# Performance work log

Hardware: AMD Instinct MI355X
Metric: run time of the kernel (lower is better)

The kernel has to match this reference:

```python
import jax, jax.numpy as jnp
import numpy as np

N_NODES = 100000
N_EDGES = 1600000
NUM_GRAPHS = 128
IN_DIM, HID, NCLS = 128, 64, 10


def setup_inputs() -> dict:
    key = jax.random.key(0)
    ks = jax.random.split(key, 12)
    inp = {
        'x': jax.random.normal(ks[0], (N_NODES, IN_DIM), jnp.float32),
        'edge_index': jax.random.randint(ks[1], (2, N_EDGES), 0, N_NODES),
        'edge_weight': jax.random.uniform(ks[2], (N_EDGES,), jnp.float32),
        'batch': jnp.sort(jax.random.randint(ks[3], (N_NODES,), 0, NUM_GRAPHS)),
        'W1': jax.random.normal(ks[4], (IN_DIM, HID), jnp.float32) * 0.05,
        'b1': jnp.zeros((HID,), jnp.float32),
        'W2': jax.random.normal(ks[5], (HID, HID), jnp.float32) * 0.05,
        'b2': jnp.zeros((HID,), jnp.float32),
        'Wc1': jax.random.normal(ks[6], (HID, HID // 2), jnp.float32) * 0.05,
        'bc1': jnp.zeros((HID // 2,), jnp.float32),
        'Wc2': jax.random.normal(ks[7], (HID // 2, NCLS), jnp.float32) * 0.05,
        'bc2': jnp.zeros((NCLS,), jnp.float32),
    }
    return inp


def _gcn_conv(x, row, col, ew, W, b, n):
    # PyG GCNConv: add self-loops (weight 1), symmetric normalization,
    # transform then aggregate: out[col] += norm * (xW)[row]
    loop = jnp.arange(n)
    r = jnp.concatenate([row, loop])
    c = jnp.concatenate([col, loop])
    w = jnp.concatenate([ew, jnp.ones((n,), ew.dtype)])
    deg = jax.ops.segment_sum(w, c, num_segments=n)
    dinv = jnp.where(deg > 0, jax.lax.rsqrt(deg), 0.0)
    norm = dinv[r] * w * dinv[c]          # [E+N]
    h = x @ W                              # [N, out]
    msg = h[r] * norm[:, None]             # [E+N, out]
    out = jax.ops.segment_sum(msg, c, num_segments=n)
    return out + b


def reference(x, edge_index, edge_weight, batch, W1, b1, W2, b2, Wc1, bc1, Wc2, bc2):
    n = x.shape[0]
    row, col = edge_index[0], edge_index[1]
    h = jax.nn.relu(_gcn_conv(x, row, col, edge_weight, W1, b1, n))
    # dropout p=0.5 is identity in eval mode
    h = jax.nn.relu(_gcn_conv(h, row, col, edge_weight, W2, b2, n))
    # global mean pool over batch indices
    sums = jax.ops.segment_sum(h, batch, num_segments=NUM_GRAPHS)
    cnts = jax.ops.segment_sum(jnp.ones((n,), h.dtype), batch, num_segments=NUM_GRAPHS)
    pooled = sums / jnp.clip(cnts, 1.0)[:, None]   # [G, HID]
    z = jax.nn.relu(pooled @ Wc1 + bc1)
    return z @ Wc2 + bc2                            # [G, NCLS]
```

## Files before the change

### kernel.cpp

```cpp
#include <hip/hip_runtime.h>
#include <hip/hip_fp16.h>


#define TPB 256
#define FIX_SCALE 16777216.0f
#define BKT_BITS 8
#define PART_BLOCKS 256

typedef _Float16 f16x8 __attribute__((ext_vector_type(8)));
typedef float f32x4 __attribute__((ext_vector_type(4)));

__device__ __forceinline__ int lower_bound_i(const int* __restrict__ a, int n, int key) {
    int lo = 0, hi = n;
    while (lo < hi) {
        int mid = (lo + hi) >> 1;
        if (a[mid] < key) lo = mid + 1; else hi = mid;
    }
    return lo;
}

__global__ __launch_bounds__(256) void k_histA(const int* __restrict__ col, int E, int CH,
                                               int K, int* __restrict__ bh,
                                               const float* __restrict__ W1,
                                               const float* __restrict__ W2,
                                               __half* __restrict__ Wt1,
                                               __half* __restrict__ Wt2) {
    __shared__ int hist[512];
    int b = blockIdx.x, t = threadIdx.x;
    if (b == 0) {
        for (int i = t; i < 64 * 128; i += 256) {
            int c = i >> 7, k = i & 127;
            Wt1[i] = (__half)W1[k * 64 + c];
        }
        for (int i = t; i < 64 * 64; i += 256) {
            int c = i >> 6, k = i & 63;
            Wt2[i] = (__half)W2[k * 64 + c];
        }
    }
    for (int i = t; i < K; i += 256) hist[i] = 0;
    __syncthreads();
    int s = b * CH, e = min(E, s + CH);
    for (int i = s + t; i < e; i += 256) atomicAdd(&hist[col[i] >> BKT_BITS], 1);
    __syncthreads();
    for (int i = t; i < K; i += 256) bh[i * PART_BLOCKS + b] = hist[i];
}

__global__ void k_scan_partial(const int* __restrict__ cnt, int* __restrict__ bsums, int n) {
    __shared__ int red[4];
    int b = blockIdx.x, t = threadIdx.x;
    int base = b * 1024;
    int s = 0;
#pragma unroll
    for (int i = 0; i < 4; i++) {
        int idx = base + t + i * TPB;
        if (idx < n) s += cnt[idx];
    }
#pragma unroll
    for (int off = 32; off > 0; off >>= 1) s += __shfl_down(s, off);
    if ((t & 63) == 0) red[t >> 6] = s;
    __syncthreads();
    if (t == 0) bsums[b] = red[0] + red[1] + red[2] + red[3];
}

__global__ void k_scan_final2(const int* __restrict__ cnt, const int* __restrict__ bsums,
                              int* __restrict__ offs, int n, int nb) {
    __shared__ int ts[TPB];
    int b = blockIdx.x, t = threadIdx.x;
    int pre = (t < b) ? bsums[t] : 0;
    ts[t] = pre; __syncthreads();
    for (int off = 128; off > 0; off >>= 1) {
        if (t < off) ts[t] += ts[t + off];
        __syncthreads();
    }
    int boff = ts[0];
    __syncthreads();

    int base = b * 1024 + 4 * t;
    int v[4]; int s = 0;
#pragma unroll
    for (int i = 0; i < 4; i++) {
        int idx = base + i;
        v[i] = (idx < n) ? cnt[idx] : 0;
        s += v[i];
    }
    ts[t] = s; __syncthreads();
    for (int off = 1; off < 256; off <<= 1) {
        int x = (t >= off) ? ts[t - off] : 0;
        __syncthreads();
        ts[t] += x;
        __syncthreads();
    }
    int run = ts[t] - s + boff;
#pragma unroll
    for (int i = 0; i < 4; i++) {
        int idx = base + i;
        if (idx < n) offs[idx] = run;
        run += v[i];
    }
}

__global__ __launch_bounds__(256) void k_partB(const int* __restrict__ row,
                                               const int* __restrict__ col,
                                               const float* __restrict__ ew,
                                               const int* __restrict__ bhs,
                                               int E, int CH, int K,
                                               int2* __restrict__ part2) {
    __shared__ int cur[512];
    int b = blockIdx.x, t = threadIdx.x;
    for (int i = t; i < K; i += 256) cur[i] = bhs[i * PART_BLOCKS + b];
    __syncthreads();
    int s = b * CH, e = min(E, s + CH);
    for (int i = s + t; i < e; i += 256) {
        int c = col[i];
        int pos = atomicAdd(&cur[c >> BKT_BITS], 1);
        part2[pos] = make_int2(row[i] | ((c & 255) << 20), __float_as_int(ew[i]));
    }
}

__global__ __launch_bounds__(256) void k_csrC(const int2* __restrict__ part2,
                                              const int* __restrict__ bhs,
                                              int K, int N, int E,
                                              int* __restrict__ offs, int* __restrict__ cnt,
                                              float* __restrict__ dinv,
                                              int2* __restrict__ csr) {
    __shared__ int lcnt[256];
    __shared__ unsigned lew[256];
    __shared__ int lcur[256];
    __shared__ int ts[256];
    int k = blockIdx.x, t = threadIdx.x;
    int n0 = k << BKT_BITS;
    lcnt[t] = 0; lew[t] = 0;
    __syncthreads();
    int estart = bhs[k * PART_BLOCKS];
    int eend   = (k + 1 < K) ? bhs[(k + 1) * PART_BLOCKS] : E;
    for (int i = estart + t; i < eend; i += 256) {
        int2 v = part2[i];
        int c = (v.x >> 20) & 255;
        atomicAdd(&lcnt[c], 1);
        float w = __int_as_float(v.y);
        atomicAdd(&lew[c], (unsigned)(w * FIX_SCALE + 0.5f));
    }
    __syncthreads();
    int myc = lcnt[t];
    ts[t] = myc; __syncthreads();
    for (int off = 1; off < 256; off <<= 1) {
        int x = (t >= off) ? ts[t - off] : 0;
        __syncthreads();
        ts[t] += x;
        __syncthreads();
    }
    int goff = estart + ts[t] - myc;
    int node = n0 + t;
    if (node < N) {
        offs[node] = goff;
        cnt[node]  = myc;
        float deg = 1.0f + (float)((double)lew[t] * (1.0 / 16777216.0));
        dinv[node] = 1.0f / sqrtf(deg);
    }
    lcur[t] = goff;
    __syncthreads();
    for (int i = estart + t; i < eend; i += 256) {
        int2 v = part2[i];
        int c = (v.x >> 20) & 255;
        int pos = atomicAdd(&lcur[c], 1);
        csr[pos] = make_int2(v.x & 0xFFFFF, v.y);
    }
}

template <int K, bool FP32IN>
__global__ __launch_bounds__(256) void k_matmul_mfma(const void* __restrict__ Xv,
                                                     const __half* __restrict__ Wt,
                                                     const float* __restrict__ dinv,
                                                     __half* __restrict__ Hh, int n) {
    const int l = threadIdx.x & 63;
    const int w = threadIdx.x >> 6;
    const int rowBase = blockIdx.x * 64 + w * 16;
    const int r = l & 15;
    const int q = l >> 4;
    const int arow = rowBase + r;
    const bool rv = arow < n;

    f32x4 acc[4] = {{0.f, 0.f, 0.f, 0.f}, {0.f, 0.f, 0.f, 0.f},
                    {0.f, 0.f, 0.f, 0.f}, {0.f, 0.f, 0.f, 0.f}};

#pragma unroll
    for (int k0 = 0; k0 < K; k0 += 32) {
        f16x8 a = {};
        if (rv) {
            if constexpr (FP32IN) {
                const float* X = (const float*)Xv;
                const float4 x0 = *reinterpret_cast<const float4*>(&X[(size_t)arow * K + k0 + 8 * q]);
                const float4 x1 = *reinterpret_cast<const float4*>(&X[(size_t)arow * K + k0 + 8 * q + 4]);
                a[0] = (_Float16)x0.x; a[1] = (_Float16)x0.y;
                a[2] = (_Float16)x0.z; a[3] = (_Float16)x0.w;
                a[4] = (_Float16)x1.x; a[5] = (_Float16)x1.y;
                a[6] = (_Float16)x1.z; a[7] = (_Float16)x1.w;
            } else {
                const _Float16* X = (const _Float16*)Xv;
                a = *reinterpret_cast<const f16x8*>(&X[(size_t)arow * K + k0 + 8 * q]);
            }
        }
#pragma unroll
        for (int ct = 0; ct < 4; ct++) {
            const f16x8 b = *reinterpret_cast<const f16x8*>(
                &Wt[(size_t)(ct * 16 + r) * K + k0 + 8 * q]);
            acc[ct] = __builtin_amdgcn_mfma_f32_16x16x32_f16(a, b, acc[ct], 0, 0, 0);
        }
    }

#pragma unroll
    for (int i = 0; i < 4; i++) {
        int r2 = rowBase + 4 * q + i;
        if (r2 < n) {
            float dv = dinv[r2];
#pragma unroll
            for (int ct = 0; ct < 4; ct++)
                Hh[(size_t)r2 * 64 + ct * 16 + r] = (__half)(acc[ct][i] * dv);
        }
    }
}

__global__ __launch_bounds__(256) void k_aggregate(
    const __half2* __restrict__ hp2, const int* __restrict__ offs,
    const int* __restrict__ cnt, const int2* __restrict__ csr,
    const float* __restrict__ dinv, const float* __restrict__ bias,
    __half2* __restrict__ outh, int n) {
    const int lane = threadIdx.x & 63;
    const int epar = lane >> 5;
    const int lpos = lane & 31;
    const int node = blockIdx.x * 4 + (threadIdx.x >> 6);
    if (node >= n) return;
    const int c = cnt[node];
    const int s = offs[node];

    int2 mc = make_int2(node, 0);
    if (lane < c) mc = csr[s + lane];
    const int cc = min(c, 64);
    const int npairs = (cc + 1) >> 1;
    const int p8 = (npairs + 7) & ~7;

    float ax[8] = {0.f, 0.f, 0.f, 0.f, 0.f, 0.f, 0.f, 0.f};
    float ay[8] = {0.f, 0.f, 0.f, 0.f, 0.f, 0.f, 0.f, 0.f};

    for (int p = 0; p < p8; p += 8) {
#pragma unroll
        for (int i = 0; i < 8; i++) {
            int idx = 2 * (p + i) + epar;
            int src = __shfl(mc.x, idx);
            float w = __int_as_float(__shfl(mc.y, idx));
            float2 f = __half22float2(hp2[(size_t)src * 32 + lpos]);
            ax[i] = fmaf(f.x, w, ax[i]);
            ay[i] = fmaf(f.y, w, ay[i]);
        }
    }
    float tx = ((ax[0] + ax[1]) + (ax[2] + ax[3])) + ((ax[4] + ax[5]) + (ax[6] + ax[7]));
    float ty = ((ay[0] + ay[1]) + (ay[2] + ay[3])) + ((ay[4] + ay[5]) + (ay[6] + ay[7]));
    tx += __shfl(tx, lane ^ 32);
    ty += __shfl(ty, lane ^ 32);

    for (int j = 64; j < c; ++j) {
        int2 e = csr[s + j];
        float2 f = __half22float2(hp2[(size_t)e.x * 32 + lpos]);
        float w = __int_as_float(e.y);
        tx = fmaf(f.x, w, tx);
        ty = fmaf(f.y, w, ty);
    }

    if (epar == 0) {
        float2 sv = __half22float2(hp2[(size_t)node * 32 + lpos]);
        const float2 bv = *reinterpret_cast<const float2*>(&bias[lpos * 2]);
        float dv = dinv[node];
        float rx = fmaxf(fmaf(tx + sv.x, dv, bv.x), 0.f);
        float ry = fmaxf(fmaf(ty + sv.y, dv, bv.y), 0.f);
        outh[(size_t)node * 32 + lpos] = __floats2half2_rn(rx, ry);
    }
}

__global__ __launch_bounds__(256) void k_pool4(
    const __half* __restrict__ oh, const int* __restrict__ batch, int n,
    float* __restrict__ psum) {
    const int g = blockIdx.x >> 2;
    const int sl = blockIdx.x & 3;
    const int t = threadIdx.x;
    const int lane = t & 63, w = t >> 6;
    __shared__ float sums[4][64];

    int start = lower_bound_i(batch, n, g);
    int end   = lower_bound_i(batch, n, g + 1);
    int len   = end - start;
    int s0 = start + (len * sl) / 4;
    int s1 = start + (len * (sl + 1)) / 4;

    float acc = 0.f;
    for (int i = s0 + w; i < s1; i += 4)
        acc += __half2float(oh[(size_t)i * 64 + lane]);
    sums[w][lane] = acc;
    __syncthreads();
    if (w == 0) {
        float v = sums[0][lane] + sums[1][lane] + sums[2][lane] + sums[3][lane];
        psum[(size_t)blockIdx.x * 64 + lane] = v;
    }
}

__global__ __launch_bounds__(64) void k_head(
    const float* __restrict__ psum, const int* __restrict__ batch, int n,
    const float* __restrict__ Wc1, const float* __restrict__ bc1,
    const float* __restrict__ Wc2, const float* __restrict__ bc2,
    float* __restrict__ out) {
    const int g = blockIdx.x;
    const int t = threadIdx.x;
    __shared__ float pooled[64];
    __shared__ float z[32];

    int start = lower_bound_i(batch, n, g);
    int end   = lower_bound_i(batch, n, g + 1);
    float ccount = (float)(end - start);

    float v = psum[(size_t)(g * 4 + 0) * 64 + t] + psum[(size_t)(g * 4 + 1) * 64 + t] +
              psum[(size_t)(g * 4 + 2) * 64 + t] + psum[(size_t)(g * 4 + 3) * 64 + t];
    pooled[t] = v / fmaxf(ccount, 1.0f);
    __syncthreads();
    if (t < 32) {
        float a = bc1[t];
#pragma unroll
        for (int k = 0; k < 64; k++) a = fmaf(pooled[k], Wc1[k * 32 + t], a);
        z[t] = fmaxf(a, 0.f);
    }
    __syncthreads();
    if (t < 10) {
        float a = bc2[t];
#pragma unroll
        for (int k = 0; k < 32; k++) a = fmaf(z[k], Wc2[k * 10 + t], a);
        out[g * 10 + t] = a;
    }
}

extern "C" void kernel_launch(void* const* d_in, const int* in_sizes, int n_in,
                              void* d_out, int out_size, void* d_ws, size_t ws_size,
                              hipStream_t stream) {
    const float* x    = (const float*)d_in[0];
    const int*   ei   = (const int*)d_in[1];
    const float* ew   = (const float*)d_in[2];
    const int*   bat  = (const int*)d_in[3];
    const float* W1   = (const float*)d_in[4];
    const float* b1   = (const float*)d_in[5];
    const float* W2   = (const float*)d_in[6];
    const float* b2   = (const float*)d_in[7];
    const float* Wc1  = (const float*)d_in[8];
    const float* bc1  = (const float*)d_in[9];
    const float* Wc2  = (const float*)d_in[10];
    const float* bc2  = (const float*)d_in[11];
    float* out = (float*)d_out;

    const int N = in_sizes[0] / 128;
    const int E = in_sizes[2];
    const int G = out_size / 10;
    const int K = (N + 255) >> BKT_BITS;
    const int KB = K * PART_BLOCKS;
    const int CH = (E + PART_BLOCKS - 1) / PART_BLOCKS;

    const int* row = ei;
    const int* col = ei + E;

    char* p = (char*)d_ws;
    auto alloc = [&](size_t bytes) -> void* {
        void* r = (void*)p;
        p += (bytes + 255) & ~(size_t)255;
        return r;
    };
    int*    bh    = (int*)   alloc((size_t)KB * 4);
    int*    bhs   = (int*)   alloc((size_t)KB * 4);
    int*    bsums = (int*)   alloc(8192);
    int*    offs  = (int*)   alloc((size_t)N * 4);
    int*    cnt   = (int*)   alloc((size_t)N * 4);
    float*  dinv  = (float*) alloc((size_t)N * 4);
    __half* Wt1   = (__half*)alloc(64 * 128 * 2);
    __half* Wt2   = (__half*)alloc(64 * 64 * 2);
    float*  psum  = (float*) alloc((size_t)G * 4 * 64 * 4);
    int2*   csr   = (int2*)  alloc((size_t)E * 8);
    size_t hbytes = (size_t)N * 64 * 2;
    size_t pbytes = (size_t)E * 8;
    char*   hbase = (char*)  alloc(hbytes > pbytes ? hbytes : pbytes);
    __half* o     = (__half*)alloc((size_t)N * 64 * 2);
    int2*   part2 = (int2*)  hbase;
    __half* h     = (__half*)hbase;

    const int NB = (KB + 1023) / 1024;
    const int gb_mm = (N + 63) / 64;
    const int gb_ag = (N + 3) / 4;

    k_histA<<<PART_BLOCKS, 256, 0, stream>>>(col, E, CH, K, bh, W1, W2, Wt1, Wt2);
    k_scan_partial<<<NB, TPB, 0, stream>>>(bh, bsums, KB);
    k_scan_final2<<<NB, TPB, 0, stream>>>(bh, bsums, bhs, KB, NB);
    k_partB<<<PART_BLOCKS, 256, 0, stream>>>(row, col, ew, bhs, E, CH, K, part2);
    k_csrC<<<K, 256, 0, stream>>>(part2, bhs, K, N, E, offs, cnt, dinv, csr);

    k_matmul_mfma<128, true><<<gb_mm, 256, 0, stream>>>(x, Wt1, dinv, h, N);
    k_aggregate<<<gb_ag, 256, 0, stream>>>((const __half2*)h, offs, cnt, csr, dinv, b1,
                                           (__half2*)o, N);
    k_matmul_mfma<64, false><<<gb_mm, 256, 0, stream>>>(o, Wt2, dinv, h, N);
    k_aggregate<<<gb_ag, 256, 0, stream>>>((const __half2*)h, offs, cnt, csr, dinv, b2,
                                           (__half2*)o, N);
    k_pool4<<<G * 4, 256, 0, stream>>>(o, bat, N, psum);
    k_head<<<G, 64, 0, stream>>>(psum, bat, N, Wc1, bc1, Wc2, bc2, out);
}
```

Measured before the change: 199.6 us.

## Fuse CSR build stages and first matmul into one cooperative kernel

Merges histogram, two-pass scan, partition, CSR construction and the first feature matmul into a single cooperative kernel launched with 512 blocks, separated by grid-wide syncs. This removes five kernel launches and their inter-kernel gaps. In exchange, the matmul now runs as a grid-stride loop over 512 resident blocks instead of a full-size grid. Each phase also idles most blocks, since only 256 or K blocks do work, and grid.sync adds its own cost.

```diff
diff --git a/kernel.cpp b/kernel.cpp
--- a/kernel.cpp
+++ b/kernel.cpp
@@ -1,11 +1,15 @@
 #include <hip/hip_runtime.h>
 #include <hip/hip_fp16.h>
+#include <hip/hip_cooperative_groups.h>
+
+namespace cg = cooperative_groups;
 
 
 #define TPB 256
 #define FIX_SCALE 16777216.0f
 #define BKT_BITS 8
 #define PART_BLOCKS 256
+#define BUILD_BLOCKS 512
 
 typedef _Float16 f16x8 __attribute__((ext_vector_type(8)));
 typedef float f32x4 __attribute__((ext_vector_type(4)));
@@ -19,162 +23,15 @@
     return lo;
 }
 
-__global__ __launch_bounds__(256) void k_histA(const int* __restrict__ col, int E, int CH,
-                                               int K, int* __restrict__ bh,
-                                               const float* __restrict__ W1,
-                                               const float* __restrict__ W2,
-                                               __half* __restrict__ Wt1,
-                                               __half* __restrict__ Wt2) {
-    __shared__ int hist[512];
-    int b = blockIdx.x, t = threadIdx.x;
-    if (b == 0) {
-        for (int i = t; i < 64 * 128; i += 256) {
-            int c = i >> 7, k = i & 127;
-            Wt1[i] = (__half)W1[k * 64 + c];
-        }
-        for (int i = t; i < 64 * 64; i += 256) {
-            int c = i >> 6, k = i & 63;
-            Wt2[i] = (__half)W2[k * 64 + c];
-        }
-    }
-    for (int i = t; i < K; i += 256) hist[i] = 0;
-    __syncthreads();
-    int s = b * CH, e = min(E, s + CH);
-    for (int i = s + t; i < e; i += 256) atomicAdd(&hist[col[i] >> BKT_BITS], 1);
-    __syncthreads();
-    for (int i = t; i < K; i += 256) bh[i * PART_BLOCKS + b] = hist[i];
-}
-
-__global__ void k_scan_partial(const int* __restrict__ cnt, int* __restrict__ bsums, int n) {
-    __shared__ int red[4];
-    int b = blockIdx.x, t = threadIdx.x;
-    int base = b * 1024;
-    int s = 0;
-#pragma unroll
-    for (int i = 0; i < 4; i++) {
-        int idx = base + t + i * TPB;
-        if (idx < n) s += cnt[idx];
-    }
-#pragma unroll
-    for (int off = 32; off > 0; off >>= 1) s += __shfl_down(s, off);
-    if ((t & 63) == 0) red[t >> 6] = s;
-    __syncthreads();
-    if (t == 0) bsums[b] = red[0] + red[1] + red[2] + red[3];
-}
-
-__global__ void k_scan_final2(const int* __restrict__ cnt, const int* __restrict__ bsums,
-                              int* __restrict__ offs, int n, int nb) {
-    __shared__ int ts[TPB];
-    int b = blockIdx.x, t = threadIdx.x;
-    int pre = (t < b) ? bsums[t] : 0;
-    ts[t] = pre; __syncthreads();
-    for (int off = 128; off > 0; off >>= 1) {
-        if (t < off) ts[t] += ts[t + off];
-        __syncthreads();
-    }
-    int boff = ts[0];
-    __syncthreads();
-
-    int base = b * 1024 + 4 * t;
-    int v[4]; int s = 0;
-#pragma unroll
-    for (int i = 0; i < 4; i++) {
-        int idx = base + i;
-        v[i] = (idx < n) ? cnt[idx] : 0;
-        s += v[i];
-    }
-    ts[t] = s; __syncthreads();
-    for (int off = 1; off < 256; off <<= 1) {
-        int x = (t >= off) ? ts[t - off] : 0;
-        __syncthreads();
-        ts[t] += x;
-        __syncthreads();
-    }
-    int run = ts[t] - s + boff;
-#pragma unroll
-    for (int i = 0; i < 4; i++) {
-        int idx = base + i;
-        if (idx < n) offs[idx] = run;
-        run += v[i];
-    }
-}
-
-__global__ __launch_bounds__(256) void k_partB(const int* __restrict__ row,
-                                               const int* __restrict__ col,
-                                               const float* __restrict__ ew,
-                                               const int* __restrict__ bhs,
-                                               int E, int CH, int K,
-                                               int2* __restrict__ part2) {
-    __shared__ int cur[512];
-    int b = blockIdx.x, t = threadIdx.x;
-    for (int i = t; i < K; i += 256) cur[i] = bhs[i * PART_BLOCKS + b];
-    __syncthreads();
-    int s = b * CH, e = min(E, s + CH);
-    for (int i = s + t; i < e; i += 256) {
-        int c = col[i];
-        int pos = atomicAdd(&cur[c >> BKT_BITS], 1);
-        part2[pos] = make_int2(row[i] | ((c & 255) << 20), __float_as_int(ew[i]));
-    }
-}
-
-__global__ __launch_bounds__(256) void k_csrC(const int2* __restrict__ part2,
-                                              const int* __restrict__ bhs,
-                                              int K, int N, int E,
-                                              int* __restrict__ offs, int* __restrict__ cnt,
-                                              float* __restrict__ dinv,
-                                              int2* __restrict__ csr) {
-    __shared__ int lcnt[256];
-    __shared__ unsigned lew[256];
-    __shared__ int lcur[256];
-    __shared__ int ts[256];
-    int k = blockIdx.x, t = threadIdx.x;
-    int n0 = k << BKT_BITS;
-    lcnt[t] = 0; lew[t] = 0;
-    __syncthreads();
-    int estart = bhs[k * PART_BLOCKS];
-    int eend   = (k + 1 < K) ? bhs[(k + 1) * PART_BLOCKS] : E;
-    for (int i = estart + t; i < eend; i += 256) {
-        int2 v = part2[i];
-        int c = (v.x >> 20) & 255;
-        atomicAdd(&lcnt[c], 1);
-        float w = __int_as_float(v.y);
-        atomicAdd(&lew[c], (unsigned)(w * FIX_SCALE + 0.5f));
-    }
-    __syncthreads();
-    int myc = lcnt[t];
-    ts[t] = myc; __syncthreads();
-    for (int off = 1; off < 256; off <<= 1) {
-        int x = (t >= off) ? ts[t - off] : 0;
-        __syncthreads();
-        ts[t] += x;
-        __syncthreads();
-    }
-    int goff = estart + ts[t] - myc;
-    int node = n0 + t;
-    if (node < N) {
-        offs[node] = goff;
-        cnt[node]  = myc;
-        float deg = 1.0f + (float)((double)lew[t] * (1.0 / 16777216.0));
-        dinv[node] = 1.0f / sqrtf(deg);
-    }
-    lcur[t] = goff;
-    __syncthreads();
-    for (int i = estart + t; i < eend; i += 256) {
-        int2 v = part2[i];
-        int c = (v.x >> 20) & 255;
-        int pos = atomicAdd(&lcur[c], 1);
-        csr[pos] = make_int2(v.x & 0xFFFFF, v.y);
-    }
-}
-
-template <int K, bool FP32IN>
-__global__ __launch_bounds__(256) void k_matmul_mfma(const void* __restrict__ Xv,
-                                                     const __half* __restrict__ Wt,
-                                                     const float* __restrict__ dinv,
-                                                     __half* __restrict__ Hh, int n) {
-    const int l = threadIdx.x & 63;
-    const int w = threadIdx.x >> 6;
-    const int rowBase = blockIdx.x * 64 + w * 16;
+template <int KK, bool FP32IN>
+__device__ __forceinline__ void mm_body(const void* __restrict__ Xv,
+                                        const __half* __restrict__ Wt,
+                                        const float* __restrict__ dinv,
+                                        __half* __restrict__ Hh, int n,
+                                        int bid, int tid) {
+    const int l = tid & 63;
+    const int w = tid >> 6;
+    const int rowBase = bid * 64 + w * 16;
     const int r = l & 15;
     const int q = l >> 4;
     const int arow = rowBase + r;
@@ -184,26 +41,26 @@
                     {0.f, 0.f, 0.f, 0.f}, {0.f, 0.f, 0.f, 0.f}};
 
 #pragma unroll
-    for (int k0 = 0; k0 < K; k0 += 32) {
+    for (int k0 = 0; k0 < KK; k0 += 32) {
         f16x8 a = {};
         if (rv) {
             if constexpr (FP32IN) {
                 const float* X = (const float*)Xv;
-                const float4 x0 = *reinterpret_cast<const float4*>(&X[(size_t)arow * K + k0 + 8 * q]);
-                const float4 x1 = *reinterpret_cast<const float4*>(&X[(size_t)arow * K + k0 + 8 * q + 4]);
+                const float4 x0 = *reinterpret_cast<const float4*>(&X[(size_t)arow * KK + k0 + 8 * q]);
+                const float4 x1 = *reinterpret_cast<const float4*>(&X[(size_t)arow * KK + k0 + 8 * q + 4]);
                 a[0] = (_Float16)x0.x; a[1] = (_Float16)x0.y;
                 a[2] = (_Float16)x0.z; a[3] = (_Float16)x0.w;
                 a[4] = (_Float16)x1.x; a[5] = (_Float16)x1.y;
                 a[6] = (_Float16)x1.z; a[7] = (_Float16)x1.w;
             } else {
                 const _Float16* X = (const _Float16*)Xv;
-                a = *reinterpret_cast<const f16x8*>(&X[(size_t)arow * K + k0 + 8 * q]);
+                a = *reinterpret_cast<const f16x8*>(&X[(size_t)arow * KK + k0 + 8 * q]);
             }
         }
 #pragma unroll
         for (int ct = 0; ct < 4; ct++) {
             const f16x8 b = *reinterpret_cast<const f16x8*>(
-                &Wt[(size_t)(ct * 16 + r) * K + k0 + 8 * q]);
+                &Wt[(size_t)(ct * 16 + r) * KK + k0 + 8 * q]);
             acc[ct] = __builtin_amdgcn_mfma_f32_16x16x32_f16(a, b, acc[ct], 0, 0, 0);
         }
     }
@@ -218,6 +75,162 @@
                 Hh[(size_t)r2 * 64 + ct * 16 + r] = (__half)(acc[ct][i] * dv);
         }
     }
+}
+
+template <int KK, bool FP32IN>
+__global__ __launch_bounds__(256) void k_matmul_mfma(const void* __restrict__ Xv,
+                                                     const __half* __restrict__ Wt,
+                                                     const float* __restrict__ dinv,
+                                                     __half* __restrict__ Hh, int n) {
+    mm_body<KK, FP32IN>(Xv, Wt, dinv, Hh, n, blockIdx.x, threadIdx.x);
+}
+
+__global__ __launch_bounds__(256) void k_build(
+    const int* __restrict__ row, const int* __restrict__ col,
+    const float* __restrict__ ew, int E, int CH, int K, int KB, int NB,
+    int* __restrict__ bh, int* __restrict__ bsums, int* __restrict__ bhs,
+    int* __restrict__ offs, int* __restrict__ cnt, float* __restrict__ dinv,
+    int2* __restrict__ part2, int2* __restrict__ csr,
+    const float* __restrict__ W1, const float* __restrict__ W2,
+    __half* __restrict__ Wt1, __half* __restrict__ Wt2,
+    const float* __restrict__ X, __half* __restrict__ Hh, int N, int gbmm) {
+    cg::grid_group grid = cg::this_grid();
+    __shared__ __align__(16) int smem[1024];
+    const int b = blockIdx.x;
+    const int t = threadIdx.x;
+
+    if (b == 256) {
+        for (int i = t; i < 64 * 128; i += 256) {
+            int c = i >> 7, k = i & 127;
+            Wt1[i] = (__half)W1[k * 64 + c];
+        }
+        for (int i = t; i < 64 * 64; i += 256) {
+            int c = i >> 6, k = i & 63;
+            Wt2[i] = (__half)W2[k * 64 + c];
+        }
+    } else if (b < PART_BLOCKS) {
+        int* hist = smem;
+        for (int i = t; i < K; i += 256) hist[i] = 0;
+        __syncthreads();
+        int s = b * CH, e = min(E, s + CH);
+        for (int i = s + t; i < e; i += 256) atomicAdd(&hist[col[i] >> BKT_BITS], 1);
+        __syncthreads();
+        for (int i = t; i < K; i += 256) bh[i * PART_BLOCKS + b] = hist[i];
+    }
+    grid.sync();
+
+    if (b < NB) {
+        int* red = smem;
+        int base = b * 1024;
+        int s = 0;
+#pragma unroll
+        for (int i = 0; i < 4; i++) {
+            int idx = base + t + i * 256;
+            if (idx < KB) s += bh[idx];
+        }
+#pragma unroll
+        for (int off = 32; off > 0; off >>= 1) s += __shfl_down(s, off);
+        if ((t & 63) == 0) red[t >> 6] = s;
+        __syncthreads();
+        if (t == 0) bsums[b] = red[0] + red[1] + red[2] + red[3];
+    }
+    grid.sync();
+
+    if (b < NB) {
+        int* ts = smem;
+        int pre = (t < b) ? bsums[t] : 0;
+        ts[t] = pre; __syncthreads();
+        for (int off = 128; off > 0; off >>= 1) {
+            if (t < off) ts[t] += ts[t + off];
+            __syncthreads();
+        }
+        int boff = ts[0];
+        __syncthreads();
+        int base = b * 1024 + 4 * t;
+        int v[4]; int s = 0;
+#pragma unroll
+        for (int i = 0; i < 4; i++) {
+            int idx = base + i;
+            v[i] = (idx < KB) ? bh[idx] : 0;
+            s += v[i];
+        }
+        ts[t] = s; __syncthreads();
+        for (int off = 1; off < 256; off <<= 1) {
+            int x = (t >= off) ? ts[t - off] : 0;
+            __syncthreads();
+            ts[t] += x;
+            __syncthreads();
+        }
+        int run = ts[t] - s + boff;
+#pragma unroll
+        for (int i = 0; i < 4; i++) {
+            int idx = base + i;
+            if (idx < KB) bhs[idx] = run;
+            run += v[i];
+        }
+    }
+    grid.sync();
+
+    if (b < PART_BLOCKS) {
+        int* cur = smem;
+        for (int i = t; i < K; i += 256) cur[i] = bhs[i * PART_BLOCKS + b];
+        __syncthreads();
+        int s = b * CH, e = min(E, s + CH);
+        for (int i = s + t; i < e; i += 256) {
+            int c = col[i];
+            int pos = atomicAdd(&cur[c >> BKT_BITS], 1);
+            part2[pos] = make_int2(row[i] | ((c & 255) << 20), __float_as_int(ew[i]));
+        }
+    }
+    grid.sync();
+
+    if (b < K) {
+        int* lcnt = smem;
+        unsigned* lew = (unsigned*)(smem + 256);
+        int* lcur = smem + 512;
+        int* ts = smem + 768;
+        int n0 = b << BKT_BITS;
+        lcnt[t] = 0; lew[t] = 0;
+        __syncthreads();
+        int estart = bhs[b * PART_BLOCKS];
+        int eend   = (b + 1 < K) ? bhs[(b + 1) * PART_BLOCKS] : E;
+        for (int i = estart + t; i < eend; i += 256) {
+            int2 v = part2[i];
+            int c = (v.x >> 20) & 255;
+            atomicAdd(&lcnt[c], 1);
+            float w = __int_as_float(v.y);
+            atomicAdd(&lew[c], (unsigned)(w * FIX_SCALE + 0.5f));
+        }
+        __syncthreads();
+        int myc = lcnt[t];
+        ts[t] = myc; __syncthreads();
+        for (int off = 1; off < 256; off <<= 1) {
+            int x = (t >= off) ? ts[t - off] : 0;
+            __syncthreads();
+            ts[t] += x;
+            __syncthreads();
+        }
+        int goff = estart + ts[t] - myc;
+        int node = n0 + t;
+        if (node < N) {
+            offs[node] = goff;
+            cnt[node]  = myc;
+            float deg = 1.0f + (float)((double)lew[t] * (1.0 / 16777216.0));
+            dinv[node] = 1.0f / sqrtf(deg);
+        }
+        lcur[t] = goff;
+        __syncthreads();
+        for (int i = estart + t; i < eend; i += 256) {
+            int2 v = part2[i];
+            int c = (v.x >> 20) & 255;
+            int pos = atomicAdd(&lcur[c], 1);
+            csr[pos] = make_int2(v.x & 0xFFFFF, v.y);
+        }
+    }
+    grid.sync();
+
+    for (int tile = b; tile < gbmm; tile += (int)gridDim.x)
+        mm_body<128, true>(X, Wt1, dinv, Hh, N, tile, t);
 }
 
 __global__ __launch_bounds__(256) void k_aggregate(
@@ -358,6 +371,7 @@
     const int K = (N + 255) >> BKT_BITS;
     const int KB = K * PART_BLOCKS;
     const int CH = (E + PART_BLOCKS - 1) / PART_BLOCKS;
+    const int NB = (KB + 1023) / 1024;
 
     const int* row = ei;
     const int* col = ei + E;
@@ -369,8 +383,8 @@
         return r;
     };
     int*    bh    = (int*)   alloc((size_t)KB * 4);
+    int*    bsums = (int*)   alloc(8192);
     int*    bhs   = (int*)   alloc((size_t)KB * 4);
-    int*    bsums = (int*)   alloc(8192);
     int*    offs  = (int*)   alloc((size_t)N * 4);
     int*    cnt   = (int*)   alloc((size_t)N * 4);
     float*  dinv  = (float*) alloc((size_t)N * 4);
@@ -385,17 +399,22 @@
     int2*   part2 = (int2*)  hbase;
     __half* h     = (__half*)hbase;
 
-    const int NB = (KB + 1023) / 1024;
     const int gb_mm = (N + 63) / 64;
     const int gb_ag = (N + 3) / 4;
 
-    k_histA<<<PART_BLOCKS, 256, 0, stream>>>(col, E, CH, K, bh, W1, W2, Wt1, Wt2);
-    k_scan_partial<<<NB, TPB, 0, stream>>>(bh, bsums, KB);
-    k_scan_final2<<<NB, TPB, 0, stream>>>(bh, bsums, bhs, KB, NB);
-    k_partB<<<PART_BLOCKS, 256, 0, stream>>>(row, col, ew, bhs, E, CH, K, part2);
-    k_csrC<<<K, 256, 0, stream>>>(part2, bhs, K, N, E, offs, cnt, dinv, csr);
-
-    k_matmul_mfma<128, true><<<gb_mm, 256, 0, stream>>>(x, Wt1, dinv, h, N);
+    {
+        int gbmm = gb_mm;
+        void* args[] = {
+            (void*)&row, (void*)&col, (void*)&ew, (void*)&E, (void*)&CH,
+            (void*)&K, (void*)&KB, (void*)&NB,
+            (void*)&bh, (void*)&bsums, (void*)&bhs,
+            (void*)&offs, (void*)&cnt, (void*)&dinv,
+            (void*)&part2, (void*)&csr,
+            (void*)&W1, (void*)&W2, (void*)&Wt1, (void*)&Wt2,
+            (void*)&x, (void*)&h, (void*)&N, (void*)&gbmm};
+        hipLaunchCooperativeKernel((void*)k_build, dim3(BUILD_BLOCKS), dim3(256),
+                                   args, 0, stream);
+    }
     k_aggregate<<<gb_ag, 256, 0, stream>>>((const __half2*)h, offs, cnt, csr, dinv, b1,
                                            (__half2*)o, N);
     k_matmul_mfma<64, false><<<gb_mm, 256, 0, stream>>>(o, Wt2, dinv, h, N);
```

After: 484.8 us. 2.43x slower.
